# Kernel optimization log

Hardware: AMD Instinct MI355X
Metric: run time of the kernel (lower is better)

Reference implementation:

```python
import jax, jax.numpy as jnp
import numpy as np

M_DIM = 1024
N_HEADS = 16
H_DIM = M_DIM // N_HEADS
FFN_H = 2 * M_DIM
B, S = 2, 2048
EPS = 1e-5
NEG = -1e9


def layernorm(x, g, b):
    mu = jnp.mean(x, axis=-1, keepdims=True)
    var = jnp.mean((x - mu) ** 2, axis=-1, keepdims=True)
    return (x - mu) * jax.lax.rsqrt(var + EPS) * g + b


def setup_inputs() -> dict:
    key = jax.random.key(0)
    ks = jax.random.split(key, 16)
    sc = 0.02
    return {
        "x": jax.random.normal(ks[0], (B, S, M_DIM), jnp.float32),
        "attention_mask": jnp.ones((B, S), jnp.int32),
        # per-head QKV projections stacked over heads: [H, M, D]
        "Wq": jax.random.normal(ks[1], (N_HEADS, M_DIM, H_DIM), jnp.float32) * sc,
        "bq": jnp.zeros((N_HEADS, H_DIM), jnp.float32),
        "Wk": jax.random.normal(ks[2], (N_HEADS, M_DIM, H_DIM), jnp.float32) * sc,
        "bk": jnp.zeros((N_HEADS, H_DIM), jnp.float32),
        "Wv": jax.random.normal(ks[3], (N_HEADS, M_DIM, H_DIM), jnp.float32) * sc,
        "bv": jnp.zeros((N_HEADS, H_DIM), jnp.float32),
        "Wo": jax.random.normal(ks[4], (M_DIM, M_DIM), jnp.float32) * sc,
        "bo": jnp.zeros((M_DIM,), jnp.float32),
        "g1": jnp.ones((M_DIM,), jnp.float32),
        "b1": jnp.zeros((M_DIM,), jnp.float32),
        "W1": jax.random.normal(ks[5], (M_DIM, FFN_H), jnp.float32) * sc,
        "bias1": jnp.zeros((FFN_H,), jnp.float32),
        "W2": jax.random.normal(ks[6], (FFN_H, M_DIM), jnp.float32) * sc,
        "bias2": jnp.zeros((M_DIM,), jnp.float32),
        "g2": jnp.ones((M_DIM,), jnp.float32),
        "b2": jnp.zeros((M_DIM,), jnp.float32),
    }


def reference(x, attention_mask, Wq, bq, Wk, bk, Wv, bv, Wo, bo, g1, b1, W1, bias1, W2, bias2, g2, b2):
    # All heads at once (the torch code loops over heads; same math).
    q = jnp.einsum("bsm,hmd->bhsd", x, Wq) + bq[None, :, None, :]
    k = jnp.einsum("bsm,hmd->bhsd", x, Wk) + bk[None, :, None, :]
    v = jnp.einsum("bsm,hmd->bhsd", x, Wv) + bv[None, :, None, :]
    scores = jnp.einsum("bhqd,bhkd->bhqk", q, k) / jnp.sqrt(jnp.float32(H_DIM))
    mask = attention_mask[:, None, None, :].astype(bool)  # [B,1,1,S] over keys
    scores = jnp.where(mask, scores, NEG)
    attn = jax.nn.softmax(scores, axis=-1)
    ctx = jnp.einsum("bhqk,bhkd->bhqd", attn, v)
    ctx = ctx.transpose(0, 2, 1, 3).reshape(x.shape[0], x.shape[1], M_DIM)  # concat heads
    out = ctx @ Wo + bo
    out = layernorm(out + x, g1, b1)
    fout = jax.nn.relu(out @ W1 + bias1) @ W2 + bias2
    out = layernorm(out + fout, g2, b2)
    return out
```

## Files before the change

### kernel.cpp

```cpp
#include <hip/hip_runtime.h>

#define MDIM 1024
#define FFH  2048
#define SEQ  2048
#define AST  72
#define VST  136
#define QSCL 0.18033688f

#if __has_builtin(__builtin_amdgcn_exp2f)
  #define EXP2(x) __builtin_amdgcn_exp2f(x)
#else
  #define EXP2(x) exp2f(x)
#endif

typedef __attribute__((ext_vector_type(8))) __bf16 bf16x8;
typedef __attribute__((ext_vector_type(4))) float floatx4;
typedef __attribute__((address_space(3))) unsigned int lds_uint;
typedef const __attribute__((address_space(1))) unsigned int g_uint;

__device__ __forceinline__ unsigned short f2bf(float f){
  union { float f; unsigned u; } v; v.f = f;
  unsigned u = v.u;
  u += 0x7fffu + ((u >> 16) & 1u);
  return (unsigned short)(u >> 16);
}
__device__ __forceinline__ unsigned short f2bf_tr(float f){
  union { float f; unsigned u; } v; v.f = f;
  return (unsigned short)(v.u >> 16);
}

__global__ void k_cvt_qb(const float* __restrict__ x, unsigned short* __restrict__ xb,
                         const float* __restrict__ bq, const float* __restrict__ bk,
                         const float* __restrict__ bv, float* __restrict__ qbias){
  const int bid = blockIdx.x, t = threadIdx.x;
  if (bid < 4096){
    int i = (bid * 256 + t) * 4;
    float4 v = *(const float4*)(x + i);
    ushort4 o;
    o.x = f2bf(v.x); o.y = f2bf(v.y); o.z = f2bf(v.z); o.w = f2bf(v.w);
    *(ushort4*)(xb + i) = o;
  } else {
    int i = (bid - 4096) * 256 + t;
    qbias[i] = (i < 1024) ? bq[i] * QSCL : (i < 2048) ? bk[i - 1024] : bv[i - 2048];
  }
}

__global__ void __launch_bounds__(256) k_prep_w(const float* __restrict__ Wo, const float* __restrict__ W1,
                                                const float* __restrict__ W2, const float* __restrict__ Wq,
                                                const float* __restrict__ Wk, const float* __restrict__ Wv,
                                                unsigned short* __restrict__ wot, unsigned short* __restrict__ w1t,
                                                unsigned short* __restrict__ w2t, unsigned short* __restrict__ wqkvt){
  __shared__ unsigned short Ts[32 * 36];
  const int t = threadIdx.x, bid = blockIdx.x;
  const int lr = t >> 3, lc4 = (t & 7) << 2;
  if (bid >= 5120){
    const int id = bid - 5120;
    const int xm = id & 31, yd = (id >> 5) & 1, z = id >> 6;
    const int tensor = z >> 4, h = z & 15;
    const float* W = (tensor == 0) ? Wq : (tensor == 1) ? Wk : Wv;
    const float scl = (tensor == 0) ? QSCL : 1.0f;
    const int m0 = xm << 5, d0 = yd << 5;
    float4 v = *(const float4*)(W + ((size_t)h << 16) + (size_t)(m0 + lr) * 64 + d0 + lc4);
    ushort4 o; o.x = f2bf(v.x * scl); o.y = f2bf(v.y * scl); o.z = f2bf(v.z * scl); o.w = f2bf(v.w * scl);
    *(ushort4*)&Ts[lr * 36 + lc4] = o;
    __syncthreads();
    ushort4 w;
    w.x = Ts[(lc4 + 0) * 36 + lr];
    w.y = Ts[(lc4 + 1) * 36 + lr];
    w.z = Ts[(lc4 + 2) * 36 + lr];
    w.w = Ts[(lc4 + 3) * 36 + lr];
    const int n = (tensor << 10) + (h << 6) + d0 + lr;
    *(ushort4*)(wqkvt + ((size_t)n << 10) + m0 + lc4) = w;
    return;
  }
  const float* src; unsigned short* dst; int K, N, k0, n0;
  if (bid < 1024){
    src = Wo; dst = wot; K = 1024; N = 1024;
    n0 = (bid & 31) << 5; k0 = (bid >> 5) << 5;
  } else if (bid < 3072){
    const int id = bid - 1024;
    src = W1; dst = w1t; K = 1024; N = 2048;
    n0 = (id & 63) << 5; k0 = (id >> 6) << 5;
  } else {
    const int id = bid - 3072;
    src = W2; dst = w2t; K = 2048; N = 1024;
    n0 = (id & 31) << 5; k0 = (id >> 5) << 5;
  }
  float4 v = *(const float4*)(src + (size_t)(k0 + lr) * N + n0 + lc4);
  ushort4 o; o.x = f2bf(v.x); o.y = f2bf(v.y); o.z = f2bf(v.z); o.w = f2bf(v.w);
  *(ushort4*)&Ts[lr * 36 + lc4] = o;
  __syncthreads();
  ushort4 w;
  w.x = Ts[(lc4 + 0) * 36 + lr];
  w.y = Ts[(lc4 + 1) * 36 + lr];
  w.z = Ts[(lc4 + 2) * 36 + lr];
  w.w = Ts[(lc4 + 3) * 36 + lr];
  *(ushort4*)(dst + (size_t)(n0 + lr) * K + k0 + lc4) = w;
}

template<int RELU, int OUTBF>
__global__ void __launch_bounds__(256) k_gemm128(const unsigned short* __restrict__ A,
                                                 const unsigned short* __restrict__ Bt,
                                                 const float* __restrict__ bias,
                                                 void* __restrict__ Cout, int N, int K){
  __shared__ unsigned short As[2 * 128 * 32];
  __shared__ unsigned short Bs[2 * 128 * 32];
  const int t = threadIdx.x;
  const int m0 = blockIdx.y << 7, n0 = blockIdx.x << 7;
  const int lane = t & 63, w = t >> 6;
  const int quad = lane >> 4, l16 = lane & 15;
  const int mw = (w & 1) << 6, nw = (w >> 1) << 6;
  floatx4 acc[4][4];
  #pragma unroll
  for (int i = 0; i < 4; i++)
    #pragma unroll
    for (int j = 0; j < 4; j++) acc[i][j] = (floatx4){0.f, 0.f, 0.f, 0.f};
  const unsigned short* Ag  = A  + (size_t)(m0 + (t >> 2)) * K + ((t & 3) << 3);
  const unsigned short* Ag2 = Ag + (size_t)64 * K;
  const unsigned short* Bg  = Bt + (size_t)(n0 + (t >> 2)) * K + ((t & 3) << 3);
  const unsigned short* Bg2 = Bg + (size_t)64 * K;
  for (int kb = 0; kb < K; kb += 64){
    #pragma unroll
    for (int s = 0; s < 2; s++){
      const int ko = kb + (s << 5), lo = (s << 12) + (t << 3);
      __builtin_amdgcn_global_load_lds((g_uint*)(Ag  + ko), (lds_uint*)&As[lo],        16, 0, 0);
      __builtin_amdgcn_global_load_lds((g_uint*)(Ag2 + ko), (lds_uint*)&As[lo + 2048], 16, 0, 0);
      __builtin_amdgcn_global_load_lds((g_uint*)(Bg  + ko), (lds_uint*)&Bs[lo],        16, 0, 0);
      __builtin_amdgcn_global_load_lds((g_uint*)(Bg2 + ko), (lds_uint*)&Bs[lo + 2048], 16, 0, 0);
    }
    __syncthreads();
    #pragma unroll
    for (int s = 0; s < 2; s++){
      const int sb = s << 12;
      bf16x8 af[4], bf[4];
      #pragma unroll
      for (int mt = 0; mt < 4; mt++)
        af[mt] = *(const bf16x8*)&As[sb + ((mw + (mt << 4) + l16) << 5) + (quad << 3)];
      #pragma unroll
      for (int nt = 0; nt < 4; nt++)
        bf[nt] = *(const bf16x8*)&Bs[sb + ((nw + (nt << 4) + l16) << 5) + (quad << 3)];
      #pragma unroll
      for (int mt = 0; mt < 4; mt++)
        #pragma unroll
        for (int nt = 0; nt < 4; nt++)
          acc[mt][nt] = __builtin_amdgcn_mfma_f32_16x16x32_bf16(af[mt], bf[nt], acc[mt][nt], 0, 0, 0);
    }
    __syncthreads();
  }
  #pragma unroll
  for (int nt = 0; nt < 4; nt++){
    const int col = n0 + nw + (nt << 4) + l16;
    const float bsv = bias[col];
    #pragma unroll
    for (int mt = 0; mt < 4; mt++){
      const int row = m0 + mw + (mt << 4) + (quad << 2);
      #pragma unroll
      for (int r = 0; r < 4; r++){
        float v = acc[mt][nt][r] + bsv;
        if (RELU) v = fmaxf(v, 0.f);
        if (OUTBF) ((unsigned short*)Cout)[(size_t)(row + r) * N + col] = f2bf(v);
        else       ((float*)Cout)[(size_t)(row + r) * N + col] = v;
      }
    }
  }
}

template<int RELU, int OUTBF>
__global__ void __launch_bounds__(256) k_gemm64n(const unsigned short* __restrict__ A,
                                                 const unsigned short* __restrict__ Bt,
                                                 const float* __restrict__ bias,
                                                 void* __restrict__ Cout, int N, int K){
  __shared__ unsigned short As[2 * 128 * 32];
  __shared__ unsigned short Bs[2 * 64 * 32];
  const int t = threadIdx.x;
  const int m0 = blockIdx.y << 7, n0 = blockIdx.x << 6;
  const int lane = t & 63, w = t >> 6;
  const int quad = lane >> 4, l16 = lane & 15;
  const int mw = (w & 1) << 6, nw = (w >> 1) << 5;
  floatx4 acc[4][2];
  #pragma unroll
  for (int i = 0; i < 4; i++)
    #pragma unroll
    for (int j = 0; j < 2; j++) acc[i][j] = (floatx4){0.f, 0.f, 0.f, 0.f};
  const unsigned short* Ag  = A  + (size_t)(m0 + (t >> 2)) * K + ((t & 3) << 3);
  const unsigned short* Ag2 = Ag + (size_t)64 * K;
  const unsigned short* Bg  = Bt + (size_t)(n0 + (t >> 2)) * K + ((t & 3) << 3);
  for (int kb = 0; kb < K; kb += 64){
    #pragma unroll
    for (int s = 0; s < 2; s++){
      const int ko = kb + (s << 5);
      __builtin_amdgcn_global_load_lds((g_uint*)(Ag  + ko), (lds_uint*)&As[(s << 12) + (t << 3)],        16, 0, 0);
      __builtin_amdgcn_global_load_lds((g_uint*)(Ag2 + ko), (lds_uint*)&As[(s << 12) + (t << 3) + 2048], 16, 0, 0);
      __builtin_amdgcn_global_load_lds((g_uint*)(Bg  + ko), (lds_uint*)&Bs[(s << 11) + (t << 3)],        16, 0, 0);
    }
    __syncthreads();
    #pragma unroll
    for (int s = 0; s < 2; s++){
      bf16x8 af[4], bf[2];
      #pragma unroll
      for (int mt = 0; mt < 4; mt++)
        af[mt] = *(const bf16x8*)&As[(s << 12) + ((mw + (mt << 4) + l16) << 5) + (quad << 3)];
      #pragma unroll
      for (int nt = 0; nt < 2; nt++)
        bf[nt] = *(const bf16x8*)&Bs[(s << 11) + ((nw + (nt << 4) + l16) << 5) + (quad << 3)];
      #pragma unroll
      for (int mt = 0; mt < 4; mt++)
        #pragma unroll
        for (int nt = 0; nt < 2; nt++)
          acc[mt][nt] = __builtin_amdgcn_mfma_f32_16x16x32_bf16(af[mt], bf[nt], acc[mt][nt], 0, 0, 0);
    }
    __syncthreads();
  }
  #pragma unroll
  for (int nt = 0; nt < 2; nt++){
    const int col = n0 + nw + (nt << 4) + l16;
    const float bsv = bias[col];
    #pragma unroll
    for (int mt = 0; mt < 4; mt++){
      const int row = m0 + mw + (mt << 4) + (quad << 2);
      #pragma unroll
      for (int r = 0; r < 4; r++){
        float v = acc[mt][nt][r] + bsv;
        if (RELU) v = fmaxf(v, 0.f);
        if (OUTBF) ((unsigned short*)Cout)[(size_t)(row + r) * N + col] = f2bf(v);
        else       ((float*)Cout)[(size_t)(row + r) * N + col] = v;
      }
    }
  }
}

__global__ void __launch_bounds__(512, 4) k_attn(const unsigned short* __restrict__ qkvb,
                                                 const int* __restrict__ amask,
                                                 unsigned short* __restrict__ ctxb){
  __shared__ __align__(16) unsigned short Ks[128 * AST];
  __shared__ __align__(16) unsigned short Vt[64 * VST];
  __shared__ __align__(16) unsigned short PQs[128 * VST];
  __shared__ int msk[128];
  const int t = threadIdx.x;
  const int w = t >> 6, lane = t & 63;
  const int quad = lane >> 4, l16 = lane & 15;
  const int b = blockIdx.y >> 4, h = blockIdx.y & 15;
  const int q0 = blockIdx.x << 7;
  const int myrow = (w << 4) + l16;
  const int sr = t >> 2, sc = (t & 3) << 4;
  const int kg = t >> 4, dc = (t & 15) << 2;

  {
    const unsigned short* qs = qkvb + (size_t)((b << 11) + q0 + sr) * 3072 + (h << 6) + sc;
    *(uint4*)&PQs[sr * VST + sc]     = *(const uint4*)qs;
    *(uint4*)&PQs[sr * VST + sc + 8] = *(const uint4*)(qs + 8);
  }
  __syncthreads();
  const bf16x8 qf0 = *(const bf16x8*)&PQs[myrow * VST + (quad << 3)];
  const bf16x8 qf1 = *(const bf16x8*)&PQs[myrow * VST + (quad << 3) + 32];

  floatx4 accO[4];
  #pragma unroll
  for (int i = 0; i < 4; i++) accO[i] = (floatx4){0.f, 0.f, 0.f, 0.f};
  float l_run = 0.f;

  const unsigned short* kbase = qkvb + (size_t)((b << 11) + sr) * 3072 + 1024 + (h << 6) + sc;
  const unsigned short* vbase = qkvb + (size_t)((b << 11) + (kg << 2)) * 3072 + 2048 + (h << 6) + dc;
  const int* mbase = amask + (b << 11);

  uint4 krA, krB;
  ushort4 vr0, vr1, vr2, vr3;
  int mreg = 1;
  {
    const unsigned short* ks = kbase;
    krA = *(const uint4*)ks;
    krB = *(const uint4*)(ks + 8);
    const unsigned short* vs = vbase;
    vr0 = *(const ushort4*)(vs);
    vr1 = *(const ushort4*)(vs + 3072);
    vr2 = *(const ushort4*)(vs + 2 * 3072);
    vr3 = *(const ushort4*)(vs + 3 * 3072);
    if (t < 128) mreg = mbase[t];
  }

  for (int k0 = 0; k0 < SEQ; k0 += 128){
    __syncthreads();
    *(uint4*)&Ks[sr * AST + sc]     = krA;
    *(uint4*)&Ks[sr * AST + sc + 8] = krB;
    {
      ushort4 c;
      c.x = vr0.x; c.y = vr1.x; c.z = vr2.x; c.w = vr3.x; *(ushort4*)&Vt[(dc + 0) * VST + (kg << 2)] = c;
      c.x = vr0.y; c.y = vr1.y; c.z = vr2.y; c.w = vr3.y; *(ushort4*)&Vt[(dc + 1) * VST + (kg << 2)] = c;
      c.x = vr0.z; c.y = vr1.z; c.z = vr2.z; c.w = vr3.z; *(ushort4*)&Vt[(dc + 2) * VST + (kg << 2)] = c;
      c.x = vr0.w; c.y = vr1.w; c.z = vr2.w; c.w = vr3.w; *(ushort4*)&Vt[(dc + 3) * VST + (kg << 2)] = c;
    }
    if (t < 128) msk[t] = mreg;
    __syncthreads();
    if (k0 + 128 < SEQ){
      const unsigned short* ks = kbase + (size_t)(k0 + 128) * 3072;
      krA = *(const uint4*)ks;
      krB = *(const uint4*)(ks + 8);
      const unsigned short* vs = vbase + (size_t)(k0 + 128) * 3072;
      vr0 = *(const ushort4*)(vs);
      vr1 = *(const ushort4*)(vs + 3072);
      vr2 = *(const ushort4*)(vs + 2 * 3072);
      vr3 = *(const ushort4*)(vs + 3 * 3072);
      if (t < 128) mreg = mbase[k0 + 128 + t];
    }

    float lsum = 0.f;
    #pragma unroll
    for (int mt = 0; mt < 8; mt++){
      floatx4 st = (floatx4){0.f, 0.f, 0.f, 0.f};
      const unsigned short* kp = &Ks[((mt << 4) + l16) * AST + (quad << 3)];
      bf16x8 kf0 = *(const bf16x8*)(kp);
      bf16x8 kf1 = *(const bf16x8*)(kp + 32);
      st = __builtin_amdgcn_mfma_f32_16x16x32_bf16(kf0, qf0, st, 0, 0, 0);
      st = __builtin_amdgcn_mfma_f32_16x16x32_bf16(kf1, qf1, st, 0, 0, 0);
      const int4 m4 = *(const int4*)&msk[(mt << 4) + (quad << 2)];
      float p0 = m4.x ? EXP2(st[0]) : 0.f;
      float p1 = m4.y ? EXP2(st[1]) : 0.f;
      float p2 = m4.z ? EXP2(st[2]) : 0.f;
      float p3 = m4.w ? EXP2(st[3]) : 0.f;
      lsum += p0 + p1 + p2 + p3;
      ushort4 o;
      o.x = f2bf_tr(p0); o.y = f2bf_tr(p1); o.z = f2bf_tr(p2); o.w = f2bf_tr(p3);
      *(ushort4*)&PQs[myrow * VST + (mt << 4) + (quad << 2)] = o;
    }
    lsum += __shfl_xor(lsum, 16);
    lsum += __shfl_xor(lsum, 32);
    l_run += lsum;
    asm volatile("" ::: "memory");
    bf16x8 pf[4];
    #pragma unroll
    for (int s = 0; s < 4; s++)
      pf[s] = *(const bf16x8*)&PQs[myrow * VST + (s << 5) + (quad << 3)];
    #pragma unroll
    for (int mt = 0; mt < 4; mt++){
      const unsigned short* vp = &Vt[((mt << 4) + l16) * VST + (quad << 3)];
      #pragma unroll
      for (int s = 0; s < 4; s++){
        bf16x8 vf = *(const bf16x8*)(vp + (s << 5));
        accO[mt] = __builtin_amdgcn_mfma_f32_16x16x32_bf16(vf, pf[s], accO[mt], 0, 0, 0);
      }
    }
  }
  const float linv = 1.f / l_run;
  unsigned short* orow = ctxb + (size_t)((b << 11) + q0 + myrow) * 1024 + (h << 6);
  #pragma unroll
  for (int mt = 0; mt < 4; mt++){
    ushort4 o;
    o.x = f2bf(accO[mt][0] * linv);
    o.y = f2bf(accO[mt][1] * linv);
    o.z = f2bf(accO[mt][2] * linv);
    o.w = f2bf(accO[mt][3] * linv);
    *(ushort4*)&orow[(mt << 4) + (quad << 2)] = o;
  }
}

__global__ void __launch_bounds__(256) k_ln(const unsigned short* __restrict__ a,
                                            const float* __restrict__ res,
                                            const float* __restrict__ gg, const float* __restrict__ bb,
                                            float* __restrict__ out, unsigned short* __restrict__ outb){
  const int row = blockIdx.x, t = threadIdx.x;
  const ushort4 au = ((const ushort4*)(a + (size_t)row * 1024))[t];
  const float4 rv = ((const float4*)(res + (size_t)row * 1024))[t];
  float4 v;
  { union { unsigned u; float f; } c;
    c.u = (unsigned)au.x << 16; v.x = c.f + rv.x;
    c.u = (unsigned)au.y << 16; v.y = c.f + rv.y;
    c.u = (unsigned)au.z << 16; v.z = c.f + rv.z;
    c.u = (unsigned)au.w << 16; v.w = c.f + rv.w; }
  float sum = v.x + v.y + v.z + v.w;
  float ss  = v.x * v.x + v.y * v.y + v.z * v.z + v.w * v.w;
  #pragma unroll
  for (int off = 32; off > 0; off >>= 1){
    sum += __shfl_down(sum, off);
    ss  += __shfl_down(ss, off);
  }
  __shared__ float red[8];
  const int w = t >> 6;
  if ((t & 63) == 0){ red[w] = sum; red[4 + w] = ss; }
  __syncthreads();
  const float S  = red[0] + red[1] + red[2] + red[3];
  const float SS = red[4] + red[5] + red[6] + red[7];
  const float mu  = S * (1.f / 1024.f);
  const float var = SS * (1.f / 1024.f) - mu * mu;
  const float rs  = rsqrtf(var + 1e-5f);
  const float4 gv = ((const float4*)gg)[t];
  const float4 bv = ((const float4*)bb)[t];
  float4 o;
  o.x = (v.x - mu) * rs * gv.x + bv.x;
  o.y = (v.y - mu) * rs * gv.y + bv.y;
  o.z = (v.z - mu) * rs * gv.z + bv.z;
  o.w = (v.w - mu) * rs * gv.w + bv.w;
  ((float4*)(out + (size_t)row * 1024))[t] = o;
  if (outb){
    ushort4 ob; ob.x = f2bf(o.x); ob.y = f2bf(o.y); ob.z = f2bf(o.z); ob.w = f2bf(o.w);
    ((ushort4*)(outb + (size_t)row * 1024))[t] = ob;
  }
}

extern "C" void kernel_launch(void* const* d_in, const int* in_sizes, int n_in,
                              void* d_out, int out_size, void* d_ws, size_t ws_size,
                              hipStream_t stream){
  const float* x     = (const float*)d_in[0];
  const int*   amask = (const int*)d_in[1];
  const float* Wq    = (const float*)d_in[2];
  const float* bq    = (const float*)d_in[3];
  const float* Wk    = (const float*)d_in[4];
  const float* bk    = (const float*)d_in[5];
  const float* Wv    = (const float*)d_in[6];
  const float* bv    = (const float*)d_in[7];
  const float* Wo    = (const float*)d_in[8];
  const float* bo    = (const float*)d_in[9];
  const float* g1    = (const float*)d_in[10];
  const float* b1    = (const float*)d_in[11];
  const float* W1    = (const float*)d_in[12];
  const float* bias1 = (const float*)d_in[13];
  const float* W2    = (const float*)d_in[14];
  const float* bias2 = (const float*)d_in[15];
  const float* g2    = (const float*)d_in[16];
  const float* b2    = (const float*)d_in[17];

  char* ws = (char*)d_ws;
  unsigned short* xb    = (unsigned short*)(ws + 0);
  unsigned short* wqkvt = (unsigned short*)(ws + 8388608);
  float*          qbias = (float*)         (ws + 14680064);
  unsigned short* wot   = (unsigned short*)(ws + 14692352);
  unsigned short* w1t   = (unsigned short*)(ws + 16789504);
  unsigned short* w2t   = (unsigned short*)(ws + 20983808);
  unsigned short* ctxb  = (unsigned short*)(ws + 25178112);
  unsigned short* attnb = (unsigned short*)(ws + 33566720);
  unsigned short* fbufb = attnb;
  unsigned short* qkvb  = (unsigned short*)(ws + 50343936);
  float*          out1  = (float*)         (ws + 50343936);
  unsigned short* out1b = (unsigned short*)(ws + 50343936 + 25165824);
  unsigned short* h1    = (unsigned short*)(ws + 50343936 + 33554432);

  k_cvt_qb<<<dim3(4108), dim3(256), 0, stream>>>(x, xb, bq, bk, bv, qbias);
  k_prep_w<<<dim3(8192), dim3(256), 0, stream>>>(Wo, W1, W2, Wq, Wk, Wv, wot, w1t, w2t, wqkvt);

  k_gemm128<0,1><<<dim3(24, 32), dim3(256), 0, stream>>>(xb, wqkvt, qbias, qkvb, 3072, 1024);
  k_attn<<<dim3(16, 32), dim3(512), 0, stream>>>(qkvb, amask, ctxb);
  k_gemm64n<0,1><<<dim3(16, 32), dim3(256), 0, stream>>>(ctxb, wot, bo, attnb, MDIM, 1024);
  k_ln<<<dim3(4096), dim3(256), 0, stream>>>(attnb, x, g1, b1, out1, out1b);
  k_gemm128<1,1><<<dim3(16, 32), dim3(256), 0, stream>>>(out1b, w1t, bias1, h1, FFH, 1024);
  k_gemm64n<0,1><<<dim3(16, 32), dim3(256), 0, stream>>>(h1, w2t, bias2, fbufb, MDIM, 2048);
  k_ln<<<dim3(4096), dim3(256), 0, stream>>>(fbufb, out1, g2, b2, (float*)d_out, nullptr);
}
```

Measured before the change: 337.4 us.

## Process two query tiles per wave in attention with half the threads

The attention kernel now runs 256 threads per block, with each wave computing two 16-row query tiles. Each K and V fragment read from shared memory is reused across both tiles, and each thread stages twice as much K/V per iteration. The MFMA sections are wrapped in s_setprio to favour matrix issue. This cuts LDS reads per FLOP, but it doubles register pressure and halves the number of resident waves, which reduces latency hiding.

New measurement: 327.8 us. 1.03x faster.

```diff
diff --git a/kernel.cpp b/kernel.cpp
--- a/kernel.cpp
+++ b/kernel.cpp
@@ -229,7 +229,7 @@
   }
 }
 
-__global__ void __launch_bounds__(512, 4) k_attn(const unsigned short* __restrict__ qkvb,
+__global__ void __launch_bounds__(256, 2) k_attn(const unsigned short* __restrict__ qkvb,
                                                  const int* __restrict__ amask,
                                                  unsigned short* __restrict__ ctxb){
   __shared__ __align__(16) unsigned short Ks[128 * AST];
@@ -241,115 +241,172 @@
   const int quad = lane >> 4, l16 = lane & 15;
   const int b = blockIdx.y >> 4, h = blockIdx.y & 15;
   const int q0 = blockIdx.x << 7;
-  const int myrow = (w << 4) + l16;
+  const int r0 = (w << 5) + l16;
+  const int r1 = r0 + 16;
   const int sr = t >> 2, sc = (t & 3) << 4;
   const int kg = t >> 4, dc = (t & 15) << 2;
 
   {
-    const unsigned short* qs = qkvb + (size_t)((b << 11) + q0 + sr) * 3072 + (h << 6) + sc;
-    *(uint4*)&PQs[sr * VST + sc]     = *(const uint4*)qs;
-    *(uint4*)&PQs[sr * VST + sc + 8] = *(const uint4*)(qs + 8);
+    const unsigned short* qs = qkvb + (size_t)((b << 11) + q0 + (t >> 1)) * 3072 + (h << 6) + ((t & 1) << 5);
+    unsigned short* qd = &PQs[(t >> 1) * VST + ((t & 1) << 5)];
+    *(uint4*)(qd)      = *(const uint4*)(qs);
+    *(uint4*)(qd + 8)  = *(const uint4*)(qs + 8);
+    *(uint4*)(qd + 16) = *(const uint4*)(qs + 16);
+    *(uint4*)(qd + 24) = *(const uint4*)(qs + 24);
   }
   __syncthreads();
-  const bf16x8 qf0 = *(const bf16x8*)&PQs[myrow * VST + (quad << 3)];
-  const bf16x8 qf1 = *(const bf16x8*)&PQs[myrow * VST + (quad << 3) + 32];
-
-  floatx4 accO[4];
-  #pragma unroll
-  for (int i = 0; i < 4; i++) accO[i] = (floatx4){0.f, 0.f, 0.f, 0.f};
-  float l_run = 0.f;
-
-  const unsigned short* kbase = qkvb + (size_t)((b << 11) + sr) * 3072 + 1024 + (h << 6) + sc;
-  const unsigned short* vbase = qkvb + (size_t)((b << 11) + (kg << 2)) * 3072 + 2048 + (h << 6) + dc;
+  const bf16x8 qa0 = *(const bf16x8*)&PQs[r0 * VST + (quad << 3)];
+  const bf16x8 qa1 = *(const bf16x8*)&PQs[r0 * VST + (quad << 3) + 32];
+  const bf16x8 qb0 = *(const bf16x8*)&PQs[r1 * VST + (quad << 3)];
+  const bf16x8 qb1 = *(const bf16x8*)&PQs[r1 * VST + (quad << 3) + 32];
+
+  floatx4 accA[4], accB[4];
+  #pragma unroll
+  for (int i = 0; i < 4; i++){
+    accA[i] = (floatx4){0.f, 0.f, 0.f, 0.f};
+    accB[i] = (floatx4){0.f, 0.f, 0.f, 0.f};
+  }
+  float l_runA = 0.f, l_runB = 0.f;
+
+  const unsigned short* kbase  = qkvb + (size_t)((b << 11) + sr) * 3072 + 1024 + (h << 6) + sc;
+  const unsigned short* kbase2 = kbase + (size_t)64 * 3072;
+  const unsigned short* vbase  = qkvb + (size_t)((b << 11) + (kg << 2)) * 3072 + 2048 + (h << 6) + dc;
+  const unsigned short* vbase2 = vbase + (size_t)64 * 3072;
   const int* mbase = amask + (b << 11);
 
-  uint4 krA, krB;
-  ushort4 vr0, vr1, vr2, vr3;
+  uint4 krA, krB, krC, krD;
+  ushort4 va0, va1, va2, va3, vb0, vb1, vb2, vb3;
   int mreg = 1;
   {
-    const unsigned short* ks = kbase;
-    krA = *(const uint4*)ks;
-    krB = *(const uint4*)(ks + 8);
-    const unsigned short* vs = vbase;
-    vr0 = *(const ushort4*)(vs);
-    vr1 = *(const ushort4*)(vs + 3072);
-    vr2 = *(const ushort4*)(vs + 2 * 3072);
-    vr3 = *(const ushort4*)(vs + 3 * 3072);
+    krA = *(const uint4*)kbase;
+    krB = *(const uint4*)(kbase + 8);
+    krC = *(const uint4*)kbase2;
+    krD = *(const uint4*)(kbase2 + 8);
+    va0 = *(const ushort4*)(vbase);
+    va1 = *(const ushort4*)(vbase + 3072);
+    va2 = *(const ushort4*)(vbase + 2 * 3072);
+    va3 = *(const ushort4*)(vbase + 3 * 3072);
+    vb0 = *(const ushort4*)(vbase2);
+    vb1 = *(const ushort4*)(vbase2 + 3072);
+    vb2 = *(const ushort4*)(vbase2 + 2 * 3072);
+    vb3 = *(const ushort4*)(vbase2 + 3 * 3072);
     if (t < 128) mreg = mbase[t];
   }
 
   for (int k0 = 0; k0 < SEQ; k0 += 128){
     __syncthreads();
-    *(uint4*)&Ks[sr * AST + sc]     = krA;
-    *(uint4*)&Ks[sr * AST + sc + 8] = krB;
+    *(uint4*)&Ks[sr * AST + sc]            = krA;
+    *(uint4*)&Ks[sr * AST + sc + 8]        = krB;
+    *(uint4*)&Ks[(sr + 64) * AST + sc]     = krC;
+    *(uint4*)&Ks[(sr + 64) * AST + sc + 8] = krD;
     {
       ushort4 c;
-      c.x = vr0.x; c.y = vr1.x; c.z = vr2.x; c.w = vr3.x; *(ushort4*)&Vt[(dc + 0) * VST + (kg << 2)] = c;
-      c.x = vr0.y; c.y = vr1.y; c.z = vr2.y; c.w = vr3.y; *(ushort4*)&Vt[(dc + 1) * VST + (kg << 2)] = c;
-      c.x = vr0.z; c.y = vr1.z; c.z = vr2.z; c.w = vr3.z; *(ushort4*)&Vt[(dc + 2) * VST + (kg << 2)] = c;
-      c.x = vr0.w; c.y = vr1.w; c.z = vr2.w; c.w = vr3.w; *(ushort4*)&Vt[(dc + 3) * VST + (kg << 2)] = c;
+      c.x = va0.x; c.y = va1.x; c.z = va2.x; c.w = va3.x; *(ushort4*)&Vt[(dc + 0) * VST + (kg << 2)] = c;
+      c.x = va0.y; c.y = va1.y; c.z = va2.y; c.w = va3.y; *(ushort4*)&Vt[(dc + 1) * VST + (kg << 2)] = c;
+      c.x = va0.z; c.y = va1.z; c.z = va2.z; c.w = va3.z; *(ushort4*)&Vt[(dc + 2) * VST + (kg << 2)] = c;
+      c.x = va0.w; c.y = va1.w; c.z = va2.w; c.w = va3.w; *(ushort4*)&Vt[(dc + 3) * VST + (kg << 2)] = c;
+      c.x = vb0.x; c.y = vb1.x; c.z = vb2.x; c.w = vb3.x; *(ushort4*)&Vt[(dc + 0) * VST + ((kg + 16) << 2)] = c;
+      c.x = vb0.y; c.y = vb1.y; c.z = vb2.y; c.w = vb3.y; *(ushort4*)&Vt[(dc + 1) * VST + ((kg + 16) << 2)] = c;
+      c.x = vb0.z; c.y = vb1.z; c.z = vb2.z; c.w = vb3.z; *(ushort4*)&Vt[(dc + 2) * VST + ((kg + 16) << 2)] = c;
+      c.x = vb0.w; c.y = vb1.w; c.z = vb2.w; c.w = vb3.w; *(ushort4*)&Vt[(dc + 3) * VST + ((kg + 16) << 2)] = c;
     }
     if (t < 128) msk[t] = mreg;
     __syncthreads();
     if (k0 + 128 < SEQ){
-      const unsigned short* ks = kbase + (size_t)(k0 + 128) * 3072;
+      const unsigned short* ks  = kbase  + (size_t)(k0 + 128) * 3072;
+      const unsigned short* ks2 = kbase2 + (size_t)(k0 + 128) * 3072;
       krA = *(const uint4*)ks;
       krB = *(const uint4*)(ks + 8);
-      const unsigned short* vs = vbase + (size_t)(k0 + 128) * 3072;
-      vr0 = *(const ushort4*)(vs);
-      vr1 = *(const ushort4*)(vs + 3072);
-      vr2 = *(const ushort4*)(vs + 2 * 3072);
-      vr3 = *(const ushort4*)(vs + 3 * 3072);
+      krC = *(const uint4*)ks2;
+      krD = *(const uint4*)(ks2 + 8);
+      const unsigned short* vs  = vbase  + (size_t)(k0 + 128) * 3072;
+      const unsigned short* vs2 = vbase2 + (size_t)(k0 + 128) * 3072;
+      va0 = *(const ushort4*)(vs);
+      va1 = *(const ushort4*)(vs + 3072);
+      va2 = *(const ushort4*)(vs + 2 * 3072);
+      va3 = *(const ushort4*)(vs + 3 * 3072);
+      vb0 = *(const ushort4*)(vs2);
+      vb1 = *(const ushort4*)(vs2 + 3072);
+      vb2 = *(const ushort4*)(vs2 + 2 * 3072);
+      vb3 = *(const ushort4*)(vs2 + 3 * 3072);
       if (t < 128) mreg = mbase[k0 + 128 + t];
     }
 
-    float lsum = 0.f;
+    float lsA = 0.f, lsB = 0.f;
     #pragma unroll
     for (int mt = 0; mt < 8; mt++){
-      floatx4 st = (floatx4){0.f, 0.f, 0.f, 0.f};
       const unsigned short* kp = &Ks[((mt << 4) + l16) * AST + (quad << 3)];
-      bf16x8 kf0 = *(const bf16x8*)(kp);
-      bf16x8 kf1 = *(const bf16x8*)(kp + 32);
-      st = __builtin_amdgcn_mfma_f32_16x16x32_bf16(kf0, qf0, st, 0, 0, 0);
-      st = __builtin_amdgcn_mfma_f32_16x16x32_bf16(kf1, qf1, st, 0, 0, 0);
+      const bf16x8 kf0 = *(const bf16x8*)(kp);
+      const bf16x8 kf1 = *(const bf16x8*)(kp + 32);
+      floatx4 sA = (floatx4){0.f, 0.f, 0.f, 0.f};
+      floatx4 sB = (floatx4){0.f, 0.f, 0.f, 0.f};
+      __builtin_amdgcn_s_setprio(1);
+      sA = __builtin_amdgcn_mfma_f32_16x16x32_bf16(kf0, qa0, sA, 0, 0, 0);
+      sA = __builtin_amdgcn_mfma_f32_16x16x32_bf16(kf1, qa1, sA, 0, 0, 0);
+      sB = __builtin_amdgcn_mfma_f32_16x16x32_bf16(kf0, qb0, sB, 0, 0, 0);
+      sB = __builtin_amdgcn_mfma_f32_16x16x32_bf16(kf1, qb1, sB, 0, 0, 0);
+      __builtin_amdgcn_s_setprio(0);
       const int4 m4 = *(const int4*)&msk[(mt << 4) + (quad << 2)];
-      float p0 = m4.x ? EXP2(st[0]) : 0.f;
-      float p1 = m4.y ? EXP2(st[1]) : 0.f;
-      float p2 = m4.z ? EXP2(st[2]) : 0.f;
-      float p3 = m4.w ? EXP2(st[3]) : 0.f;
-      lsum += p0 + p1 + p2 + p3;
-      ushort4 o;
-      o.x = f2bf_tr(p0); o.y = f2bf_tr(p1); o.z = f2bf_tr(p2); o.w = f2bf_tr(p3);
-      *(ushort4*)&PQs[myrow * VST + (mt << 4) + (quad << 2)] = o;
-    }
-    lsum += __shfl_xor(lsum, 16);
-    lsum += __shfl_xor(lsum, 32);
-    l_run += lsum;
+      float pA0 = m4.x ? EXP2(sA[0]) : 0.f;
+      float pA1 = m4.y ? EXP2(sA[1]) : 0.f;
+      float pA2 = m4.z ? EXP2(sA[2]) : 0.f;
+      float pA3 = m4.w ? EXP2(sA[3]) : 0.f;
+      lsA += pA0 + pA1 + pA2 + pA3;
+      ushort4 oA;
+      oA.x = f2bf_tr(pA0); oA.y = f2bf_tr(pA1); oA.z = f2bf_tr(pA2); oA.w = f2bf_tr(pA3);
+      *(ushort4*)&PQs[r0 * VST + (mt << 4) + (quad << 2)] = oA;
+      float pB0 = m4.x ? EXP2(sB[0]) : 0.f;
+      float pB1 = m4.y ? EXP2(sB[1]) : 0.f;
+      float pB2 = m4.z ? EXP2(sB[2]) : 0.f;
+      float pB3 = m4.w ? EXP2(sB[3]) : 0.f;
+      lsB += pB0 + pB1 + pB2 + pB3;
+      ushort4 oB;
+      oB.x = f2bf_tr(pB0); oB.y = f2bf_tr(pB1); oB.z = f2bf_tr(pB2); oB.w = f2bf_tr(pB3);
+      *(ushort4*)&PQs[r1 * VST + (mt << 4) + (quad << 2)] = oB;
+    }
+    lsA += __shfl_xor(lsA, 16);
+    lsA += __shfl_xor(lsA, 32);
+    l_runA += lsA;
+    lsB += __shfl_xor(lsB, 16);
+    lsB += __shfl_xor(lsB, 32);
+    l_runB += lsB;
     asm volatile("" ::: "memory");
-    bf16x8 pf[4];
-    #pragma unroll
-    for (int s = 0; s < 4; s++)
-      pf[s] = *(const bf16x8*)&PQs[myrow * VST + (s << 5) + (quad << 3)];
+    bf16x8 pA[4], pB[4];
+    #pragma unroll
+    for (int s = 0; s < 4; s++){
+      pA[s] = *(const bf16x8*)&PQs[r0 * VST + (s << 5) + (quad << 3)];
+      pB[s] = *(const bf16x8*)&PQs[r1 * VST + (s << 5) + (quad << 3)];
+    }
     #pragma unroll
     for (int mt = 0; mt < 4; mt++){
       const unsigned short* vp = &Vt[((mt << 4) + l16) * VST + (quad << 3)];
+      __builtin_amdgcn_s_setprio(1);
       #pragma unroll
       for (int s = 0; s < 4; s++){
-        bf16x8 vf = *(const bf16x8*)(vp + (s << 5));
-        accO[mt] = __builtin_amdgcn_mfma_f32_16x16x32_bf16(vf, pf[s], accO[mt], 0, 0, 0);
+        const bf16x8 vf = *(const bf16x8*)(vp + (s << 5));
+        accA[mt] = __builtin_amdgcn_mfma_f32_16x16x32_bf16(vf, pA[s], accA[mt], 0, 0, 0);
+        accB[mt] = __builtin_amdgcn_mfma_f32_16x16x32_bf16(vf, pB[s], accB[mt], 0, 0, 0);
       }
-    }
-  }
-  const float linv = 1.f / l_run;
-  unsigned short* orow = ctxb + (size_t)((b << 11) + q0 + myrow) * 1024 + (h << 6);
+      __builtin_amdgcn_s_setprio(0);
+    }
+  }
+  const float liA = 1.f / l_runA;
+  const float liB = 1.f / l_runB;
+  unsigned short* oA = ctxb + (size_t)((b << 11) + q0 + r0) * 1024 + (h << 6);
+  unsigned short* oB = ctxb + (size_t)((b << 11) + q0 + r1) * 1024 + (h << 6);
   #pragma unroll
   for (int mt = 0; mt < 4; mt++){
     ushort4 o;
-    o.x = f2bf(accO[mt][0] * linv);
-    o.y = f2bf(accO[mt][1] * linv);
-    o.z = f2bf(accO[mt][2] * linv);
-    o.w = f2bf(accO[mt][3] * linv);
-    *(ushort4*)&orow[(mt << 4) + (quad << 2)] = o;
+    o.x = f2bf(accA[mt][0] * liA);
+    o.y = f2bf(accA[mt][1] * liA);
+    o.z = f2bf(accA[mt][2] * liA);
+    o.w = f2bf(accA[mt][3] * liA);
+    *(ushort4*)&oA[(mt << 4) + (quad << 2)] = o;
+    o.x = f2bf(accB[mt][0] * liB);
+    o.y = f2bf(accB[mt][1] * liB);
+    o.z = f2bf(accB[mt][2] * liB);
+    o.w = f2bf(accB[mt][3] * liB);
+    *(ushort4*)&oB[(mt << 4) + (quad << 2)] = o;
   }
 }
 
@@ -437,7 +494,7 @@
   k_prep_w<<<dim3(8192), dim3(256), 0, stream>>>(Wo, W1, W2, Wq, Wk, Wv, wot, w1t, w2t, wqkvt);
 
   k_gemm128<0,1><<<dim3(24, 32), dim3(256), 0, stream>>>(xb, wqkvt, qbias, qkvb, 3072, 1024);
-  k_attn<<<dim3(16, 32), dim3(512), 0, stream>>>(qkvb, amask, ctxb);
+  k_attn<<<dim3(16, 32), dim3(256), 0, stream>>>(qkvb, amask, ctxb);
   k_gemm64n<0,1><<<dim3(16, 32), dim3(256), 0, stream>>>(ctxb, wot, bo, attnb, MDIM, 1024);
   k_ln<<<dim3(4096), dim3(256), 0, stream>>>(attnb, x, g1, b1, out1, out1b);
   k_gemm128<1,1><<<dim3(16, 32), dim3(256), 0, stream>>>(out1b, w1t, bias1, h1, FFH, 1024);
```
